# Kernel optimization log

Measured on AMD Instinct MI355X. Metric: run time of the kernel, lower is better.

The kernel has to match this reference:

```python
import jax, jax.numpy as jnp
import numpy as np

VOCAB = 50000
EMBED = 128
H = 128
B, T = 64, 512
NUM_CLASSES = 10


def _lstm(h, mask, Wx, Wh, b, reverse):
    # h: [B,T,I], mask: [B,T] bool, Wx: [I,4H], Wh: [H,4H], b: [4H]
    Bb, Tt, _ = h.shape
    Hh = Wh.shape[0]
    xp = jnp.einsum('bti,ih->bth', h, Wx) + b  # [B,T,4H]

    def step(carry, inp):
        hprev, cprev = carry
        xpt, m = inp  # [B,4H], [B]
        z = xpt + hprev @ Wh
        i, f, g, o = jnp.split(z, 4, axis=-1)
        c = jax.nn.sigmoid(f) * cprev + jax.nn.sigmoid(i) * jnp.tanh(g)
        hn = jax.nn.sigmoid(o) * jnp.tanh(c)
        m = m[:, None]
        # Keras masking: masked steps carry previous output/state
        hn = jnp.where(m, hn, hprev)
        c = jnp.where(m, c, cprev)
        return (hn, c), hn

    init = (jnp.zeros((Bb, Hh), h.dtype), jnp.zeros((Bb, Hh), h.dtype))
    xs = (jnp.swapaxes(xp, 0, 1), mask.T)  # time-major
    _, ys = jax.lax.scan(step, init, xs, reverse=reverse)
    return jnp.swapaxes(ys, 0, 1)  # [B,T,H]


def _bilstm(h, mask, Wxf, Whf, bf, Wxb, Whb, bb):
    hf = _lstm(h, mask, Wxf, Whf, bf, reverse=False)
    hb = _lstm(h, mask, Wxb, Whb, bb, reverse=True)
    return jnp.concatenate([hf, hb], axis=-1)


def setup_inputs() -> dict:
    key = jax.random.key(0)
    ks = jax.random.split(key, 16)
    s = 0.05
    d = {
        'x': jax.random.randint(ks[0], (B, T), 0, VOCAB),
        'emb': jax.random.normal(ks[1], (VOCAB + 1, EMBED), jnp.float32) * s,
        'Wx_f0': jax.random.normal(ks[2], (EMBED, 4 * H), jnp.float32) * s,
        'Wh_f0': jax.random.normal(ks[3], (H, 4 * H), jnp.float32) * s,
        'b_f0': jnp.zeros((4 * H,), jnp.float32),
        'Wx_b0': jax.random.normal(ks[4], (EMBED, 4 * H), jnp.float32) * s,
        'Wh_b0': jax.random.normal(ks[5], (H, 4 * H), jnp.float32) * s,
        'b_b0': jnp.zeros((4 * H,), jnp.float32),
        'Wx_f1': jax.random.normal(ks[6], (2 * H, 4 * H), jnp.float32) * s,
        'Wh_f1': jax.random.normal(ks[7], (H, 4 * H), jnp.float32) * s,
        'b_f1': jnp.zeros((4 * H,), jnp.float32),
        'Wx_b1': jax.random.normal(ks[8], (2 * H, 4 * H), jnp.float32) * s,
        'Wh_b1': jax.random.normal(ks[9], (H, 4 * H), jnp.float32) * s,
        'b_b1': jnp.zeros((4 * H,), jnp.float32),
        'fc_W': jax.random.normal(ks[10], (2 * T, NUM_CLASSES), jnp.float32) * s,
        'fc_b': jnp.zeros((NUM_CLASSES,), jnp.float32),
    }
    return d


def reference(x, emb, Wx_f0, Wh_f0, b_f0, Wx_b0, Wh_b0, b_b0,
              Wx_f1, Wh_f1, b_f1, Wx_b1, Wh_b1, b_b1, fc_W, fc_b):
    mask = x != 0  # mask_zero=True
    h = emb[x]  # [B,T,E]
    h = _bilstm(h, mask, Wx_f0, Wh_f0, b_f0, Wx_b0, Wh_b0, b_b0)  # [B,T,2H]
    h = _bilstm(h, mask, Wx_f1, Wh_f1, b_f1, Wx_b1, Wh_b1, b_b1)  # [B,T,2H]
    # MaxPool1D/AvgPool1D with pool_size = 2H, channels_first ->
    # a single window over the whole feature axis, then Flatten -> [B,T]
    mx = jnp.max(h, axis=-1)
    av = jnp.mean(h, axis=-1)
    feat = jnp.concatenate([mx, av], axis=1)  # [B, 2T]
    return jax.nn.relu(feat @ fc_W + fc_b)
```

## Files before the change

### kernel.cpp

```cpp
#include <hip/hip_runtime.h>
#include <hip/hip_bf16.h>
#include <cstdint>
#include <cstddef>

#define B 64
#define T 512
#define EMBED 128
#define H 128
#define G4 512
#define HOUT 256
#define NUM_CLASSES 10
#define BT (B * T)

typedef float v2f __attribute__((ext_vector_type(2)));
typedef float v4f __attribute__((ext_vector_type(4)));

#define BM 128
#define BN 64
#define BK 16

__global__ __launch_bounds__(256) void gemm_bias_kernel(
    const float* __restrict__ A, const int* __restrict__ xrow,
    const float* __restrict__ W, const float* __restrict__ bias,
    float* __restrict__ C, int K)
{
    __shared__ __align__(16) float As[BK][BM + 4];
    __shared__ __align__(16) float Ws[BK][BN + 4];

    int tid = threadIdx.x;
    int tx = tid & 15;
    int ty = tid >> 4;
    int m0 = blockIdx.y * BM;
    int n0 = blockIdx.x * BN;

    int ra = tid >> 2;
    int cq = tid & 3;
    const float* arow0;
    const float* arow1;
    if (xrow) {
        arow0 = A + (size_t)xrow[m0 + ra] * K;
        arow1 = A + (size_t)xrow[m0 + ra + 64] * K;
    } else {
        arow0 = A + (size_t)(m0 + ra) * K;
        arow1 = A + (size_t)(m0 + ra + 64) * K;
    }

    float acc[8][4];
#pragma unroll
    for (int i = 0; i < 8; i++)
#pragma unroll
        for (int j = 0; j < 4; j++) acc[i][j] = 0.f;

    for (int k0 = 0; k0 < K; k0 += BK) {
        {
            float4 a = *(const float4*)&arow0[k0 + cq * 4];
            As[cq * 4 + 0][ra] = a.x;
            As[cq * 4 + 1][ra] = a.y;
            As[cq * 4 + 2][ra] = a.z;
            As[cq * 4 + 3][ra] = a.w;
            float4 b = *(const float4*)&arow1[k0 + cq * 4];
            As[cq * 4 + 0][ra + 64] = b.x;
            As[cq * 4 + 1][ra + 64] = b.y;
            As[cq * 4 + 2][ra + 64] = b.z;
            As[cq * 4 + 3][ra + 64] = b.w;
        }
        {
            int rw = tid >> 4;
            int cw = tid & 15;
            float4 wv = *(const float4*)&W[(size_t)(k0 + rw) * G4 + n0 + cw * 4];
            *(float4*)&Ws[rw][cw * 4] = wv;
        }
        __syncthreads();

#pragma unroll
        for (int k = 0; k < BK; k++) {
            float4 a0 = *(const float4*)&As[k][ty * 8];
            float4 a1 = *(const float4*)&As[k][ty * 8 + 4];
            float4 w0 = *(const float4*)&Ws[k][tx * 4];
            float av[8] = {a0.x, a0.y, a0.z, a0.w, a1.x, a1.y, a1.z, a1.w};
            float wv[4] = {w0.x, w0.y, w0.z, w0.w};
#pragma unroll
            for (int i = 0; i < 8; i++)
#pragma unroll
                for (int j = 0; j < 4; j++)
                    acc[i][j] = fmaf(av[i], wv[j], acc[i][j]);
        }
        __syncthreads();
    }

    float4 bv = *(const float4*)&bias[n0 + tx * 4];
#pragma unroll
    for (int i = 0; i < 8; i++) {
        int m = m0 + ty * 8 + i;
        float4 o;
        o.x = acc[i][0] + bv.x;
        o.y = acc[i][1] + bv.y;
        o.z = acc[i][2] + bv.z;
        o.w = acc[i][3] + bv.w;
        *(float4*)&C[(size_t)m * G4 + n0 + tx * 4] = o;
    }
}

__device__ __forceinline__ float fast_sig(float x) {
    float e = __expf(-x);
    return __builtin_amdgcn_rcpf(1.f + e);
}

template <int CTRL>
__device__ __forceinline__ float dpp_add(float x) {
    int y = __builtin_amdgcn_mov_dpp(__float_as_int(x), CTRL, 0xF, 0xF, true);
    return x + __int_as_float(y);
}

__device__ __forceinline__ void wg_barrier_lds() {
    asm volatile("s_waitcnt lgkmcnt(0)" ::: "memory");
    __builtin_amdgcn_s_barrier();
}

#define PKFMA(acc, h2, w2) \
    asm("v_pk_fma_f32 %0, %1, %2, %0" : "+v"(acc) : "v"(h2), "v"(w2))

__global__ __launch_bounds__(512) __attribute__((amdgpu_waves_per_eu(2, 2)))
void lstm_scan_kernel(
    const float* __restrict__ xp0, const float* __restrict__ xp1,
    const float* __restrict__ Wh0, const float* __restrict__ Wh1,
    const int* __restrict__ x, float* __restrict__ hout)
{
    const int b   = blockIdx.x;
    const int dir = blockIdx.y;
    const float* __restrict__ xp = dir ? xp1 : xp0;
    const float* __restrict__ Wh = dir ? Wh1 : Wh0;

    const int tid = threadIdx.x;
    const int ks  = tid & 3;
    const int q   = tid >> 2;

    const float* wp = Wh + (size_t)(ks * 32) * G4 + q;
#define LDP(c, p) v2f w##c##_##p = { wp[(2 * p) * G4 + c * H], \
                                     wp[(2 * p + 1) * G4 + c * H] }
#define DECLC(c) \
    LDP(c, 0);  LDP(c, 1);  LDP(c, 2);  LDP(c, 3);  \
    LDP(c, 4);  LDP(c, 5);  LDP(c, 6);  LDP(c, 7);  \
    LDP(c, 8);  LDP(c, 9);  LDP(c, 10); LDP(c, 11); \
    LDP(c, 12); LDP(c, 13); LDP(c, 14); LDP(c, 15);
    DECLC(0) DECLC(1) DECLC(2) DECLC(3)
#undef DECLC
#undef LDP
#define PIN4(a, b_, c_, d_) asm volatile("" : "+v"(a), "+v"(b_), "+v"(c_), "+v"(d_))
#define PINC(c) \
    PIN4(w##c##_0,  w##c##_1,  w##c##_2,  w##c##_3);  \
    PIN4(w##c##_4,  w##c##_5,  w##c##_6,  w##c##_7);  \
    PIN4(w##c##_8,  w##c##_9,  w##c##_10, w##c##_11); \
    PIN4(w##c##_12, w##c##_13, w##c##_14, w##c##_15)
    PINC(0); PINC(1); PINC(2); PINC(3);
#undef PINC
#undef PIN4

    __shared__ __align__(16) float h_sh[2][4][36];
    __shared__ unsigned char mask_sh[T];

    if (tid < H) { h_sh[0][tid >> 5][tid & 31] = 0.f; }
    mask_sh[tid] = (x[(size_t)b * T + tid] != 0) ? 1 : 0;
    float c_reg = 0.f, h_reg = 0.f;
    __syncthreads();

    const int t0 = dir ? T - 1 : 0;
    const ptrdiff_t dstep = dir ? -(ptrdiff_t)G4 : (ptrdiff_t)G4;
    const ptrdiff_t hstep = dir ? -(ptrdiff_t)HOUT : (ptrdiff_t)HOUT;
    const float* xptr = xp + ((size_t)b * T + t0) * G4 + ks * H + q;
    float*       hptr = hout + ((size_t)b * T + t0) * HOUT + dir * H + q;
    float xp_cur = *xptr;

    int cb = 0;
    int t = t0;
    const int tinc = dir ? -1 : 1;

    for (int s = 0; s < T; s++) {
        float xin = xp_cur;
        if (s + 1 < T) {
            xptr += dstep;
            xp_cur = *xptr;
        }

        v2f acc0 = { (ks == 0) ? xin : 0.f, 0.f };
        v2f acc1 = { (ks == 1) ? xin : 0.f, 0.f };
        v2f acc2 = { (ks == 2) ? xin : 0.f, 0.f };
        v2f acc3 = { (ks == 3) ? xin : 0.f, 0.f };

        const v4f* hp = (const v4f*)&h_sh[cb][ks][0];
#define STEP4(kk, pA, pB) { \
        v4f hv = hp[kk]; \
        v2f h01 = __builtin_shufflevector(hv, hv, 0, 1); \
        v2f h23 = __builtin_shufflevector(hv, hv, 2, 3); \
        PKFMA(acc0, h01, w0_##pA); PKFMA(acc0, h23, w0_##pB); \
        PKFMA(acc1, h01, w1_##pA); PKFMA(acc1, h23, w1_##pB); \
        PKFMA(acc2, h01, w2_##pA); PKFMA(acc2, h23, w2_##pB); \
        PKFMA(acc3, h01, w3_##pA); PKFMA(acc3, h23, w3_##pB); }
        STEP4(0, 0, 1)   STEP4(1, 2, 3)   STEP4(2, 4, 5)   STEP4(3, 6, 7)
        STEP4(4, 8, 9)   STEP4(5, 10, 11) STEP4(6, 12, 13) STEP4(7, 14, 15)
#undef STEP4

        float a0 = acc0.x + acc0.y;
        float a1 = acc1.x + acc1.y;
        float a2 = acc2.x + acc2.y;
        float a3 = acc3.x + acc3.y;

        a0 = dpp_add<0xB1>(a0); a1 = dpp_add<0xB1>(a1);
        a2 = dpp_add<0xB1>(a2); a3 = dpp_add<0xB1>(a3);
        a0 = dpp_add<0x4E>(a0); a1 = dpp_add<0x4E>(a1);
        a2 = dpp_add<0x4E>(a2); a3 = dpp_add<0x4E>(a3);

        float ig = fast_sig(a0);
        float fg = fast_sig(a1);
        float gg = 2.f * fast_sig(a2 + a2) - 1.f;
        float og = fast_sig(a3);
        float cn = fmaf(fg, c_reg, ig * gg);
        float th = 2.f * fast_sig(cn + cn) - 1.f;
        float hn = og * th;

        bool msk = mask_sh[t] != 0;
        c_reg = msk ? cn : c_reg;
        h_reg = msk ? hn : h_reg;

        if (ks == 0) {
            h_sh[cb ^ 1][q >> 5][q & 31] = h_reg;
            *hptr = h_reg;
        }
        hptr += hstep;
        wg_barrier_lds();
        cb ^= 1;
        t += tinc;
    }
}

__global__ __launch_bounds__(256) void pool_kernel(
    const float* __restrict__ Hin, float* __restrict__ feat)
{
    int wave = threadIdx.x >> 6;
    int lane = threadIdx.x & 63;
    int bt = blockIdx.x * 4 + wave;
    float4 v = *(const float4*)&Hin[(size_t)bt * HOUT + lane * 4];
    float mx = fmaxf(fmaxf(v.x, v.y), fmaxf(v.z, v.w));
    float sm = (v.x + v.y) + (v.z + v.w);
#pragma unroll
    for (int off = 32; off > 0; off >>= 1) {
        mx = fmaxf(mx, __shfl_down(mx, off));
        sm += __shfl_down(sm, off);
    }
    if (lane == 0) {
        int b = bt >> 9;
        int t = bt & (T - 1);
        feat[(size_t)b * (2 * T) + t]     = mx;
        feat[(size_t)b * (2 * T) + T + t] = sm * (1.f / 256.f);
    }
}

__global__ __launch_bounds__(128) void fc_kernel(
    const float* __restrict__ feat, const float* __restrict__ fcW,
    const float* __restrict__ fcb, float* __restrict__ out)
{
    __shared__ float red[2][NUM_CLASSES];
    int b = blockIdx.x, tid = threadIdx.x;
    float acc[NUM_CLASSES];
#pragma unroll
    for (int c = 0; c < NUM_CLASSES; c++) acc[c] = 0.f;
#pragma unroll
    for (int it = 0; it < 8; it++) {
        int k = tid + it * 128;
        float fv = feat[(size_t)b * 1024 + k];
#pragma unroll
        for (int c = 0; c < NUM_CLASSES; c++)
            acc[c] = fmaf(fv, fcW[(size_t)k * NUM_CLASSES + c], acc[c]);
    }
#pragma unroll
    for (int c = 0; c < NUM_CLASSES; c++) {
        float v = acc[c];
        for (int off = 32; off > 0; off >>= 1) v += __shfl_down(v, off);
        if ((tid & 63) == 0) red[tid >> 6][c] = v;
    }
    __syncthreads();
    if (tid < NUM_CLASSES) {
        float v = red[0][tid] + red[1][tid] + fcb[tid];
        out[(size_t)b * NUM_CLASSES + tid] = fmaxf(v, 0.f);
    }
}

extern "C" void kernel_launch(void* const* d_in, const int* in_sizes, int n_in,
                              void* d_out, int out_size, void* d_ws, size_t ws_size,
                              hipStream_t stream)
{
    const int*   x     = (const int*)d_in[0];
    const float* emb   = (const float*)d_in[1];
    const float* Wx_f0 = (const float*)d_in[2];
    const float* Wh_f0 = (const float*)d_in[3];
    const float* b_f0  = (const float*)d_in[4];
    const float* Wx_b0 = (const float*)d_in[5];
    const float* Wh_b0 = (const float*)d_in[6];
    const float* b_b0  = (const float*)d_in[7];
    const float* Wx_f1 = (const float*)d_in[8];
    const float* Wh_f1 = (const float*)d_in[9];
    const float* b_f1  = (const float*)d_in[10];
    const float* Wx_b1 = (const float*)d_in[11];
    const float* Wh_b1 = (const float*)d_in[12];
    const float* b_b1  = (const float*)d_in[13];
    const float* fcW   = (const float*)d_in[14];
    const float* fcb   = (const float*)d_in[15];
    float* out = (float*)d_out;

    char* ws = (char*)d_ws;
    const size_t MB = 1024 * 1024;
    float* H1   = (float*)(ws);
    float* H0   = (float*)(ws + 32 * MB);
    float* xpF  = (float*)(ws + 64 * MB);
    float* xpB  = (float*)(ws + 128 * MB);
    float* feat = (float*)(ws + 192 * MB);

    dim3 ggrid(G4 / BN, BT / BM);

    gemm_bias_kernel<<<ggrid, 256, 0, stream>>>(emb, x, Wx_f0, b_f0, xpF, EMBED);
    gemm_bias_kernel<<<ggrid, 256, 0, stream>>>(emb, x, Wx_b0, b_b0, xpB, EMBED);
    lstm_scan_kernel<<<dim3(B, 2), 512, 0, stream>>>(xpF, xpB, Wh_f0, Wh_b0, x, H0);

    gemm_bias_kernel<<<ggrid, 256, 0, stream>>>(H0, nullptr, Wx_f1, b_f1, xpF, 2 * H);
    gemm_bias_kernel<<<ggrid, 256, 0, stream>>>(H0, nullptr, Wx_b1, b_b1, xpB, 2 * H);
    lstm_scan_kernel<<<dim3(B, 2), 512, 0, stream>>>(xpF, xpB, Wh_f1, Wh_b1, x, H1);

    pool_kernel<<<BT / 4, 256, 0, stream>>>(H1, feat);
    fc_kernel<<<B, 128, 0, stream>>>(feat, fcW, fcb, out);
}
```

Before: 1.051 ms.

## Halve LSTM scan block size with two hidden units per thread

Each thread in the recurrent scan kernel now computes two hidden units (columns q0 and q0+1) instead of one, so the block shrinks from 512 to 256 threads (4 waves) and keeps twice as many weight registers (256 VGPRs of weights at one wave per EU). This halves the number of waves taking part in each per-timestep barrier and lets each LDS h-vector load feed twice as many FMAs. The cost is much higher register pressure, with a risk of spills, and a longer serial chain of work per thread on each step.

```diff
diff --git a/kernel.cpp b/kernel.cpp
--- a/kernel.cpp
+++ b/kernel.cpp
@@ -120,7 +120,7 @@
 #define PKFMA(acc, h2, w2) \
     asm("v_pk_fma_f32 %0, %1, %2, %0" : "+v"(acc) : "v"(h2), "v"(w2))
 
-__global__ __launch_bounds__(512) __attribute__((amdgpu_waves_per_eu(2, 2)))
+__global__ __launch_bounds__(256) __attribute__((amdgpu_waves_per_eu(1, 1)))
 void lstm_scan_kernel(
     const float* __restrict__ xp0, const float* __restrict__ xp1,
     const float* __restrict__ Wh0, const float* __restrict__ Wh1,
@@ -132,99 +132,126 @@
     const float* __restrict__ Wh = dir ? Wh1 : Wh0;
 
     const int tid = threadIdx.x;
-    const int ks  = tid & 3;
-    const int q   = tid >> 2;
-
-    const float* wp = Wh + (size_t)(ks * 32) * G4 + q;
-#define LDP(c, p) v2f w##c##_##p = { wp[(2 * p) * G4 + c * H], \
-                                     wp[(2 * p + 1) * G4 + c * H] }
-#define DECLC(c) \
-    LDP(c, 0);  LDP(c, 1);  LDP(c, 2);  LDP(c, 3);  \
-    LDP(c, 4);  LDP(c, 5);  LDP(c, 6);  LDP(c, 7);  \
-    LDP(c, 8);  LDP(c, 9);  LDP(c, 10); LDP(c, 11); \
-    LDP(c, 12); LDP(c, 13); LDP(c, 14); LDP(c, 15);
-    DECLC(0) DECLC(1) DECLC(2) DECLC(3)
+    const int kq  = tid & 3;
+    const int qp  = tid >> 2;
+    const int q0  = 2 * qp;
+
+    const float* wpb = Wh + (size_t)(kq * 32) * G4;
+#define LDP(P, c, p, col) v2f w##P##c##_##p = { wpb[(2 * p) * G4 + (col)], \
+                                                wpb[(2 * p + 1) * G4 + (col)] };
+#define DECLC(P, c, col) \
+    LDP(P, c, 0, col)  LDP(P, c, 1, col)  LDP(P, c, 2, col)  LDP(P, c, 3, col)  \
+    LDP(P, c, 4, col)  LDP(P, c, 5, col)  LDP(P, c, 6, col)  LDP(P, c, 7, col)  \
+    LDP(P, c, 8, col)  LDP(P, c, 9, col)  LDP(P, c, 10, col) LDP(P, c, 11, col) \
+    LDP(P, c, 12, col) LDP(P, c, 13, col) LDP(P, c, 14, col) LDP(P, c, 15, col)
+    DECLC(A, 0, 0 * H + q0) DECLC(A, 1, 1 * H + q0)
+    DECLC(A, 2, 2 * H + q0) DECLC(A, 3, 3 * H + q0)
+    DECLC(Z, 0, 0 * H + q0 + 1) DECLC(Z, 1, 1 * H + q0 + 1)
+    DECLC(Z, 2, 2 * H + q0 + 1) DECLC(Z, 3, 3 * H + q0 + 1)
 #undef DECLC
 #undef LDP
 #define PIN4(a, b_, c_, d_) asm volatile("" : "+v"(a), "+v"(b_), "+v"(c_), "+v"(d_))
-#define PINC(c) \
-    PIN4(w##c##_0,  w##c##_1,  w##c##_2,  w##c##_3);  \
-    PIN4(w##c##_4,  w##c##_5,  w##c##_6,  w##c##_7);  \
-    PIN4(w##c##_8,  w##c##_9,  w##c##_10, w##c##_11); \
-    PIN4(w##c##_12, w##c##_13, w##c##_14, w##c##_15)
-    PINC(0); PINC(1); PINC(2); PINC(3);
+#define PINC(P, c) \
+    PIN4(w##P##c##_0,  w##P##c##_1,  w##P##c##_2,  w##P##c##_3);  \
+    PIN4(w##P##c##_4,  w##P##c##_5,  w##P##c##_6,  w##P##c##_7);  \
+    PIN4(w##P##c##_8,  w##P##c##_9,  w##P##c##_10, w##P##c##_11); \
+    PIN4(w##P##c##_12, w##P##c##_13, w##P##c##_14, w##P##c##_15)
+    PINC(A, 0); PINC(A, 1); PINC(A, 2); PINC(A, 3);
+    PINC(Z, 0); PINC(Z, 1); PINC(Z, 2); PINC(Z, 3);
 #undef PINC
 #undef PIN4
 
     __shared__ __align__(16) float h_sh[2][4][36];
     __shared__ unsigned char mask_sh[T];
 
-    if (tid < H) { h_sh[0][tid >> 5][tid & 31] = 0.f; }
-    mask_sh[tid] = (x[(size_t)b * T + tid] != 0) ? 1 : 0;
-    float c_reg = 0.f, h_reg = 0.f;
+    if (tid < H) h_sh[0][tid >> 5][tid & 31] = 0.f;
+    mask_sh[tid]       = (x[(size_t)b * T + tid] != 0) ? 1 : 0;
+    mask_sh[tid + 256] = (x[(size_t)b * T + tid + 256] != 0) ? 1 : 0;
+    float cA = 0.f, hA = 0.f, cZ = 0.f, hZ = 0.f;
     __syncthreads();
 
     const int t0 = dir ? T - 1 : 0;
     const ptrdiff_t dstep = dir ? -(ptrdiff_t)G4 : (ptrdiff_t)G4;
     const ptrdiff_t hstep = dir ? -(ptrdiff_t)HOUT : (ptrdiff_t)HOUT;
-    const float* xptr = xp + ((size_t)b * T + t0) * G4 + ks * H + q;
-    float*       hptr = hout + ((size_t)b * T + t0) * HOUT + dir * H + q;
-    float xp_cur = *xptr;
+    const float* xptr = xp + ((size_t)b * T + t0) * G4 + kq * H + q0;
+    float*       hptr = hout + ((size_t)b * T + t0) * HOUT + dir * H + q0;
+    v2f xp_cur = *(const v2f*)xptr;
 
     int cb = 0;
     int t = t0;
     const int tinc = dir ? -1 : 1;
 
     for (int s = 0; s < T; s++) {
-        float xin = xp_cur;
+        v2f xin = xp_cur;
         if (s + 1 < T) {
             xptr += dstep;
-            xp_cur = *xptr;
-        }
-
-        v2f acc0 = { (ks == 0) ? xin : 0.f, 0.f };
-        v2f acc1 = { (ks == 1) ? xin : 0.f, 0.f };
-        v2f acc2 = { (ks == 2) ? xin : 0.f, 0.f };
-        v2f acc3 = { (ks == 3) ? xin : 0.f, 0.f };
-
-        const v4f* hp = (const v4f*)&h_sh[cb][ks][0];
-#define STEP4(kk, pA, pB) { \
-        v4f hv = hp[kk]; \
-        v2f h01 = __builtin_shufflevector(hv, hv, 0, 1); \
-        v2f h23 = __builtin_shufflevector(hv, hv, 2, 3); \
-        PKFMA(acc0, h01, w0_##pA); PKFMA(acc0, h23, w0_##pB); \
-        PKFMA(acc1, h01, w1_##pA); PKFMA(acc1, h23, w1_##pB); \
-        PKFMA(acc2, h01, w2_##pA); PKFMA(acc2, h23, w2_##pB); \
-        PKFMA(acc3, h01, w3_##pA); PKFMA(acc3, h23, w3_##pB); }
-        STEP4(0, 0, 1)   STEP4(1, 2, 3)   STEP4(2, 4, 5)   STEP4(3, 6, 7)
-        STEP4(4, 8, 9)   STEP4(5, 10, 11) STEP4(6, 12, 13) STEP4(7, 14, 15)
-#undef STEP4
-
-        float a0 = acc0.x + acc0.y;
-        float a1 = acc1.x + acc1.y;
-        float a2 = acc2.x + acc2.y;
-        float a3 = acc3.x + acc3.y;
-
-        a0 = dpp_add<0xB1>(a0); a1 = dpp_add<0xB1>(a1);
-        a2 = dpp_add<0xB1>(a2); a3 = dpp_add<0xB1>(a3);
-        a0 = dpp_add<0x4E>(a0); a1 = dpp_add<0x4E>(a1);
-        a2 = dpp_add<0x4E>(a2); a3 = dpp_add<0x4E>(a3);
-
-        float ig = fast_sig(a0);
-        float fg = fast_sig(a1);
-        float gg = 2.f * fast_sig(a2 + a2) - 1.f;
-        float og = fast_sig(a3);
-        float cn = fmaf(fg, c_reg, ig * gg);
-        float th = 2.f * fast_sig(cn + cn) - 1.f;
-        float hn = og * th;
+            xp_cur = *(const v2f*)xptr;
+        }
+
+        v2f aA0 = { (kq == 0) ? xin.x : 0.f, 0.f };
+        v2f aA1 = { (kq == 1) ? xin.x : 0.f, 0.f };
+        v2f aA2 = { (kq == 2) ? xin.x : 0.f, 0.f };
+        v2f aA3 = { (kq == 3) ? xin.x : 0.f, 0.f };
+        v2f aZ0 = { (kq == 0) ? xin.y : 0.f, 0.f };
+        v2f aZ1 = { (kq == 1) ? xin.y : 0.f, 0.f };
+        v2f aZ2 = { (kq == 2) ? xin.y : 0.f, 0.f };
+        v2f aZ3 = { (kq == 3) ? xin.y : 0.f, 0.f };
+
+        const v4f* hp = (const v4f*)&h_sh[cb][kq][0];
+#define BLK(kk, pA, pB) {                                                     \
+        v4f hv = hp[kk];                                                      \
+        v2f h01 = __builtin_shufflevector(hv, hv, 0, 1);                      \
+        v2f h23 = __builtin_shufflevector(hv, hv, 2, 3);                      \
+        PKFMA(aA0, h01, wA0_##pA); PKFMA(aA0, h23, wA0_##pB);                 \
+        PKFMA(aA1, h01, wA1_##pA); PKFMA(aA1, h23, wA1_##pB);                 \
+        PKFMA(aA2, h01, wA2_##pA); PKFMA(aA2, h23, wA2_##pB);                 \
+        PKFMA(aA3, h01, wA3_##pA); PKFMA(aA3, h23, wA3_##pB);                 \
+        PKFMA(aZ0, h01, wZ0_##pA); PKFMA(aZ0, h23, wZ0_##pB);                 \
+        PKFMA(aZ1, h01, wZ1_##pA); PKFMA(aZ1, h23, wZ1_##pB);                 \
+        PKFMA(aZ2, h01, wZ2_##pA); PKFMA(aZ2, h23, wZ2_##pB);                 \
+        PKFMA(aZ3, h01, wZ3_##pA); PKFMA(aZ3, h23, wZ3_##pB); }
+        BLK(0, 0, 1)   BLK(1, 2, 3)   BLK(2, 4, 5)   BLK(3, 6, 7)
+        BLK(4, 8, 9)   BLK(5, 10, 11) BLK(6, 12, 13) BLK(7, 14, 15)
+#undef BLK
+
+        float zA0 = aA0.x + aA0.y, zA1 = aA1.x + aA1.y;
+        float zA2 = aA2.x + aA2.y, zA3 = aA3.x + aA3.y;
+        float zZ0 = aZ0.x + aZ0.y, zZ1 = aZ1.x + aZ1.y;
+        float zZ2 = aZ2.x + aZ2.y, zZ3 = aZ3.x + aZ3.y;
+
+        zA0 = dpp_add<0xB1>(zA0); zA1 = dpp_add<0xB1>(zA1);
+        zA2 = dpp_add<0xB1>(zA2); zA3 = dpp_add<0xB1>(zA3);
+        zZ0 = dpp_add<0xB1>(zZ0); zZ1 = dpp_add<0xB1>(zZ1);
+        zZ2 = dpp_add<0xB1>(zZ2); zZ3 = dpp_add<0xB1>(zZ3);
+        zA0 = dpp_add<0x4E>(zA0); zA1 = dpp_add<0x4E>(zA1);
+        zA2 = dpp_add<0x4E>(zA2); zA3 = dpp_add<0x4E>(zA3);
+        zZ0 = dpp_add<0x4E>(zZ0); zZ1 = dpp_add<0x4E>(zZ1);
+        zZ2 = dpp_add<0x4E>(zZ2); zZ3 = dpp_add<0x4E>(zZ3);
+
+        float igA = fast_sig(zA0);
+        float fgA = fast_sig(zA1);
+        float ggA = 2.f * fast_sig(zA2 + zA2) - 1.f;
+        float ogA = fast_sig(zA3);
+        float cnA = fmaf(fgA, cA, igA * ggA);
+        float thA = 2.f * fast_sig(cnA + cnA) - 1.f;
+        float hnA = ogA * thA;
+
+        float igZ = fast_sig(zZ0);
+        float fgZ = fast_sig(zZ1);
+        float ggZ = 2.f * fast_sig(zZ2 + zZ2) - 1.f;
+        float ogZ = fast_sig(zZ3);
+        float cnZ = fmaf(fgZ, cZ, igZ * ggZ);
+        float thZ = 2.f * fast_sig(cnZ + cnZ) - 1.f;
+        float hnZ = ogZ * thZ;
 
         bool msk = mask_sh[t] != 0;
-        c_reg = msk ? cn : c_reg;
-        h_reg = msk ? hn : h_reg;
-
-        if (ks == 0) {
-            h_sh[cb ^ 1][q >> 5][q & 31] = h_reg;
-            *hptr = h_reg;
+        cA = msk ? cnA : cA;  hA = msk ? hnA : hA;
+        cZ = msk ? cnZ : cZ;  hZ = msk ? hnZ : hZ;
+
+        if (kq == 0) {
+            v2f hw = { hA, hZ };
+            *(v2f*)&h_sh[cb ^ 1][q0 >> 5][q0 & 31] = hw;
+            *(v2f*)hptr = hw;
         }
         hptr += hstep;
         wg_barrier_lds();
@@ -319,11 +346,11 @@
 
     gemm_bias_kernel<<<ggrid, 256, 0, stream>>>(emb, x, Wx_f0, b_f0, xpF, EMBED);
     gemm_bias_kernel<<<ggrid, 256, 0, stream>>>(emb, x, Wx_b0, b_b0, xpB, EMBED);
-    lstm_scan_kernel<<<dim3(B, 2), 512, 0, stream>>>(xpF, xpB, Wh_f0, Wh_b0, x, H0);
+    lstm_scan_kernel<<<dim3(B, 2), 256, 0, stream>>>(xpF, xpB, Wh_f0, Wh_b0, x, H0);
 
     gemm_bias_kernel<<<ggrid, 256, 0, stream>>>(H0, nullptr, Wx_f1, b_f1, xpF, 2 * H);
     gemm_bias_kernel<<<ggrid, 256, 0, stream>>>(H0, nullptr, Wx_b1, b_b1, xpB, 2 * H);
-    lstm_scan_kernel<<<dim3(B, 2), 512, 0, stream>>>(xpF, xpB, Wh_f1, Wh_b1, x, H1);
+    lstm_scan_kernel<<<dim3(B, 2), 256, 0, stream>>>(xpF, xpB, Wh_f1, Wh_b1, x, H1);
 
     pool_kernel<<<BT / 4, 256, 0, stream>>>(H1, feat);
     fc_kernel<<<B, 128, 0, stream>>>(feat, fcW, fcb, out);
```

Result: slower. 1.417 ms (+34.8%).

## Replace FP32 input-projection GEMMs with split-bf16 MFMA GEMM fusing both directions

Applied to the files above, without the earlier changes.

Each layer's two FP32 SIMT input-projection GEMMs become one bf16 MFMA GEMM covering forward and backward weights together (N=1024). FP32 accuracy is approximated by splitting each operand into bf16 hi and lo parts and summing three products (hi*hi, hi*lo, lo*hi). New prep kernels gather the embeddings or hidden states and transpose and split the weights into bf16 pairs first. This adds extra kernel launches and memory traffic and leaves a small precision loss, in exchange for matrix-core throughput on the GEMM part; the LSTM scans are unchanged.

```diff
diff --git a/kernel.cpp b/kernel.cpp
--- a/kernel.cpp
+++ b/kernel.cpp
@@ -14,90 +14,133 @@
 
 typedef float v2f __attribute__((ext_vector_type(2)));
 typedef float v4f __attribute__((ext_vector_type(4)));
-
-#define BM 128
-#define BN 64
-#define BK 16
-
-__global__ __launch_bounds__(256) void gemm_bias_kernel(
-    const float* __restrict__ A, const int* __restrict__ xrow,
-    const float* __restrict__ W, const float* __restrict__ bias,
-    float* __restrict__ C, int K)
-{
-    __shared__ __align__(16) float As[BK][BM + 4];
-    __shared__ __align__(16) float Ws[BK][BN + 4];
-
-    int tid = threadIdx.x;
-    int tx = tid & 15;
-    int ty = tid >> 4;
-    int m0 = blockIdx.y * BM;
-    int n0 = blockIdx.x * BN;
-
-    int ra = tid >> 2;
-    int cq = tid & 3;
-    const float* arow0;
-    const float* arow1;
-    if (xrow) {
-        arow0 = A + (size_t)xrow[m0 + ra] * K;
-        arow1 = A + (size_t)xrow[m0 + ra + 64] * K;
-    } else {
-        arow0 = A + (size_t)(m0 + ra) * K;
-        arow1 = A + (size_t)(m0 + ra + 64) * K;
-    }
-
-    float acc[8][4];
-#pragma unroll
-    for (int i = 0; i < 8; i++)
-#pragma unroll
-        for (int j = 0; j < 4; j++) acc[i][j] = 0.f;
-
-    for (int k0 = 0; k0 < K; k0 += BK) {
+typedef short v8s __attribute__((ext_vector_type(8)));
+
+__device__ __forceinline__ unsigned short bf16_hi(float v) {
+    return (unsigned short)(__float_as_uint(v) >> 16);
+}
+__device__ __forceinline__ unsigned short bf16_lo(float v, unsigned short hi) {
+    float hf = __uint_as_float((unsigned)hi << 16);
+    return (unsigned short)(__float_as_uint(v - hf) >> 16);
+}
+
+__global__ __launch_bounds__(128) void prep_w2t_kernel(
+    const float* __restrict__ Wf, const float* __restrict__ Wb,
+    unsigned short* __restrict__ w2t, int K)
+{
+    int n = blockIdx.x;
+    const float* src = (n < 512) ? (Wf + n) : (Wb + (n - 512));
+    unsigned short* dst = w2t + (size_t)n * (2 * K);
+    for (int j = threadIdx.x; j < K; j += 128) {
+        float v = src[(size_t)j * G4];
+        unsigned short hi = bf16_hi(v);
+        dst[j]     = hi;
+        dst[K + j] = bf16_lo(v, hi);
+    }
+}
+
+__global__ __launch_bounds__(128) void prep_a2_emb_kernel(
+    const int* __restrict__ x, const float* __restrict__ emb,
+    unsigned short* __restrict__ a2)
+{
+    int m = blockIdx.x;
+    int j = threadIdx.x;
+    float v = emb[(size_t)x[m] * EMBED + j];
+    unsigned short hi = bf16_hi(v);
+    a2[(size_t)m * 256 + j]       = hi;
+    a2[(size_t)m * 256 + 128 + j] = bf16_lo(v, hi);
+}
+
+__global__ __launch_bounds__(256) void prep_a2_h_kernel(
+    const float* __restrict__ H0, unsigned short* __restrict__ a2)
+{
+    int m = blockIdx.x;
+    int j = threadIdx.x;
+    float v = H0[(size_t)m * 256 + j];
+    unsigned short hi = bf16_hi(v);
+    a2[(size_t)m * 512 + j]       = hi;
+    a2[(size_t)m * 512 + 256 + j] = bf16_lo(v, hi);
+}
+
+__global__ __launch_bounds__(256) void gemm_mfma_kernel(
+    const unsigned short* __restrict__ a2, const unsigned short* __restrict__ w2t,
+    const float* __restrict__ bF, const float* __restrict__ bB,
+    float* __restrict__ xpF, float* __restrict__ xpB, int K)
+{
+    __shared__ __align__(16) unsigned short As[128 * 40];
+    __shared__ __align__(16) unsigned short Ws[128 * 40];
+
+    const int tid  = threadIdx.x;
+    const int lane = tid & 63;
+    const int wv   = tid >> 6;
+    const int wr   = wv >> 1;
+    const int wc   = wv & 1;
+    const int n0   = blockIdx.x * 128;
+    const int m0   = blockIdx.y * 128;
+    const int K2   = 2 * K;
+
+    const int srow  = tid >> 1;
+    const int spart = tid & 1;
+    const unsigned short* agp = a2 + (size_t)(m0 + srow) * K2 + spart * 16;
+    const unsigned short* wgp = w2t + (size_t)(n0 + srow) * K2 + spart * 16;
+    unsigned short* alp = &As[srow * 40 + spart * 16];
+    unsigned short* wlp = &Ws[srow * 40 + spart * 16];
+
+    v4f acc[4][4];
+#pragma unroll
+    for (int i = 0; i < 4; i++)
+#pragma unroll
+        for (int j = 0; j < 4; j++) acc[i][j] = (v4f){0.f, 0.f, 0.f, 0.f};
+
+    const int ksub = K >> 5;
+    const int nsteps = 3 * ksub;
+    for (int s = 0; s < nsteps; ++s) {
+        int t  = s / ksub;
+        int kk = s - t * ksub;
+        int aoff = ((t == 2) ? K : 0) + kk * 32;
+        int woff = ((t == 1) ? K : 0) + kk * 32;
+
         {
-            float4 a = *(const float4*)&arow0[k0 + cq * 4];
-            As[cq * 4 + 0][ra] = a.x;
-            As[cq * 4 + 1][ra] = a.y;
-            As[cq * 4 + 2][ra] = a.z;
-            As[cq * 4 + 3][ra] = a.w;
-            float4 b = *(const float4*)&arow1[k0 + cq * 4];
-            As[cq * 4 + 0][ra + 64] = b.x;
-            As[cq * 4 + 1][ra + 64] = b.y;
-            As[cq * 4 + 2][ra + 64] = b.z;
-            As[cq * 4 + 3][ra + 64] = b.w;
-        }
-        {
-            int rw = tid >> 4;
-            int cw = tid & 15;
-            float4 wv = *(const float4*)&W[(size_t)(k0 + rw) * G4 + n0 + cw * 4];
-            *(float4*)&Ws[rw][cw * 4] = wv;
+            v8s a0 = *(const v8s*)(agp + aoff);
+            v8s a1 = *(const v8s*)(agp + aoff + 8);
+            v8s w0 = *(const v8s*)(wgp + woff);
+            v8s w1 = *(const v8s*)(wgp + woff + 8);
+            *(v8s*)(alp)     = a0;
+            *(v8s*)(alp + 8) = a1;
+            *(v8s*)(wlp)     = w0;
+            *(v8s*)(wlp + 8) = w1;
         }
         __syncthreads();
 
-#pragma unroll
-        for (int k = 0; k < BK; k++) {
-            float4 a0 = *(const float4*)&As[k][ty * 8];
-            float4 a1 = *(const float4*)&As[k][ty * 8 + 4];
-            float4 w0 = *(const float4*)&Ws[k][tx * 4];
-            float av[8] = {a0.x, a0.y, a0.z, a0.w, a1.x, a1.y, a1.z, a1.w};
-            float wv[4] = {w0.x, w0.y, w0.z, w0.w};
-#pragma unroll
-            for (int i = 0; i < 8; i++)
-#pragma unroll
-                for (int j = 0; j < 4; j++)
-                    acc[i][j] = fmaf(av[i], wv[j], acc[i][j]);
+        v8s af[4], wf[4];
+#pragma unroll
+        for (int mr = 0; mr < 4; mr++)
+            af[mr] = *(const v8s*)&As[(wr * 64 + mr * 16 + (lane & 15)) * 40 + (lane >> 4) * 8];
+#pragma unroll
+        for (int nr = 0; nr < 4; nr++)
+            wf[nr] = *(const v8s*)&Ws[(wc * 64 + nr * 16 + (lane & 15)) * 40 + (lane >> 4) * 8];
+#pragma unroll
+        for (int mr = 0; mr < 4; mr++)
+#pragma unroll
+            for (int nr = 0; nr < 4; nr++)
+                acc[mr][nr] = __builtin_amdgcn_mfma_f32_16x16x32_bf16(
+                    af[mr], wf[nr], acc[mr][nr], 0, 0, 0);
+        __syncthreads();
+    }
+
+#pragma unroll
+    for (int nr = 0; nr < 4; nr++) {
+        int gcol = n0 + wc * 64 + nr * 16 + (lane & 15);
+        float bv = (gcol < 512) ? bF[gcol] : bB[gcol - 512];
+        float* dst = (gcol < 512) ? (xpF + gcol) : (xpB + gcol - 512);
+#pragma unroll
+        for (int mr = 0; mr < 4; mr++) {
+            int grow = m0 + wr * 64 + mr * 16 + (lane >> 4) * 4;
+            v4f fr = acc[mr][nr];
+#pragma unroll
+            for (int r = 0; r < 4; r++)
+                dst[(size_t)(grow + r) * G4] = fr[r] + bv;
         }
-        __syncthreads();
-    }
-
-    float4 bv = *(const float4*)&bias[n0 + tx * 4];
-#pragma unroll
-    for (int i = 0; i < 8; i++) {
-        int m = m0 + ty * 8 + i;
-        float4 o;
-        o.x = acc[i][0] + bv.x;
-        o.y = acc[i][1] + bv.y;
-        o.z = acc[i][2] + bv.z;
-        o.w = acc[i][3] + bv.w;
-        *(float4*)&C[(size_t)m * G4 + n0 + tx * 4] = o;
     }
 }
 
@@ -309,22 +352,25 @@
 
     char* ws = (char*)d_ws;
     const size_t MB = 1024 * 1024;
-    float* H1   = (float*)(ws);
-    float* H0   = (float*)(ws + 32 * MB);
-    float* xpF  = (float*)(ws + 64 * MB);
-    float* xpB  = (float*)(ws + 128 * MB);
-    float* feat = (float*)(ws + 192 * MB);
-
-    dim3 ggrid(G4 / BN, BT / BM);
-
-    gemm_bias_kernel<<<ggrid, 256, 0, stream>>>(emb, x, Wx_f0, b_f0, xpF, EMBED);
-    gemm_bias_kernel<<<ggrid, 256, 0, stream>>>(emb, x, Wx_b0, b_b0, xpB, EMBED);
-    lstm_scan_kernel<<<dim3(B, 2), 512, 0, stream>>>(xpF, xpB, Wh_f0, Wh_b0, x, H0);
-
-    gemm_bias_kernel<<<ggrid, 256, 0, stream>>>(H0, nullptr, Wx_f1, b_f1, xpF, 2 * H);
-    gemm_bias_kernel<<<ggrid, 256, 0, stream>>>(H0, nullptr, Wx_b1, b_b1, xpB, 2 * H);
-    lstm_scan_kernel<<<dim3(B, 2), 512, 0, stream>>>(xpF, xpB, Wh_f1, Wh_b1, x, H1);
-
-    pool_kernel<<<BT / 4, 256, 0, stream>>>(H1, feat);
+    float*          Hbuf = (float*)(ws);
+    float*          xpF  = (float*)(ws + 32 * MB);
+    float*          xpB  = (float*)(ws + 96 * MB);
+    unsigned short* a2   = (unsigned short*)(ws + 160 * MB);
+    unsigned short* w2t  = (unsigned short*)(ws + 192 * MB);
+    float*          feat = (float*)(ws + 193 * MB);
+
+    dim3 ggrid(1024 / 128, BT / 128);
+
+    prep_w2t_kernel<<<1024, 128, 0, stream>>>(Wx_f0, Wx_b0, w2t, EMBED);
+    prep_a2_emb_kernel<<<BT, 128, 0, stream>>>(x, emb, a2);
+    gemm_mfma_kernel<<<ggrid, 256, 0, stream>>>(a2, w2t, b_f0, b_b0, xpF, xpB, EMBED);
+    lstm_scan_kernel<<<dim3(B, 2), 512, 0, stream>>>(xpF, xpB, Wh_f0, Wh_b0, x, Hbuf);
+
+    prep_w2t_kernel<<<1024, 128, 0, stream>>>(Wx_f1, Wx_b1, w2t, 2 * H);
+    prep_a2_h_kernel<<<BT, 256, 0, stream>>>(Hbuf, a2);
+    gemm_mfma_kernel<<<ggrid, 256, 0, stream>>>(a2, w2t, b_f1, b_b1, xpF, xpB, 2 * H);
+    lstm_scan_kernel<<<dim3(B, 2), 512, 0, stream>>>(xpF, xpB, Wh_f1, Wh_b1, x, Hbuf);
+
+    pool_kernel<<<BT / 4, 256, 0, stream>>>(Hbuf, feat);
     fc_kernel<<<B, 128, 0, stream>>>(feat, fcW, fcb, out);
 }
```

After: 872.3 us, median of 2. 1.21x faster.
